# Optimization experiments

Measured on AMD Instinct MI355X. Metric: run time of the kernel, lower is better.

The kernel has to match this reference:

```python
import jax, jax.numpy as jnp
import numpy as np

B, D, H, Q, N, V = 2048, 2048, 16, 128, 8192, 128


def setup_inputs() -> dict:
    key = jax.random.key(0)
    k1, k2, k3, k4, k5 = jax.random.split(key, 5)
    return {
        "x": jax.random.normal(k1, (B, D), dtype=jnp.float32),
        "keys": jax.random.normal(k2, (N, Q), dtype=jnp.float32),
        "values": jax.random.normal(k3, (N, V), dtype=jnp.float32),
        "Wq": jax.random.normal(k4, (H * Q, D), dtype=jnp.float32) * (1.0 / np.sqrt(D)),
        "Wo": jax.random.normal(k5, (D, H * V), dtype=jnp.float32) * (1.0 / np.sqrt(H * V)),
    }


def reference(x, keys, values, Wq, Wo):
    b = x.shape[0]
    h, q = H, Q
    # queries: [B, H, Q]
    queries = (x @ Wq.T).reshape(b, h, q)
    # einsum 'aib,ajb->aijb' then sum over last axis == dot product over Q
    scores = jnp.einsum('bhq,nq->bhn', queries, keys) / jnp.sqrt(jnp.asarray(q, x.dtype))
    attn = jax.nn.softmax(scores, axis=-1)  # [B, H, N]
    # Original: einsum('aib,ajc->aijc', attn, values) sums attn over its N axis
    # (label b) independently of values' N axis (label j), giving
    # out[a,i,j,c] = attn_rowsum[a,i] * values[j,c]; mean over j then yields
    # attn_rowsum[a,i] * mean_n(values)[c]. Computed here without the [B,H,N,V]
    # intermediate (mathematically identical).
    attn_rowsum = attn.sum(axis=-1)        # [B, H] (== 1 up to fp error)
    vmean = values.mean(axis=0)            # [V]
    outv = (attn_rowsum[:, :, None] * vmean[None, None, :]).reshape(b, -1)  # [B, H*V]
    return outv @ Wo.T + x
```

## Files before the change

kernel.cpp:

```cpp
#include <hip/hip_runtime.h>


#define NROWS 8192
#define VDIM  128
#define DDIM  2048
#define BDIM  2048

__global__ void __launch_bounds__(256) colsum_kernel(
    const float4* __restrict__ vals4,
    float4* __restrict__ partial4)
{
    __shared__ float4 s[256];
    const int t = threadIdx.x;
    const int bid = blockIdx.x;
    float4 acc = make_float4(0.f, 0.f, 0.f, 0.f);
    const int base = bid * 4096;
#pragma unroll
    for (int j = 0; j < 16; ++j) {
        float4 v = vals4[base + t + 256 * j];
        acc.x += v.x; acc.y += v.y; acc.z += v.z; acc.w += v.w;
    }
    s[t] = acc;
    __syncthreads();
    if (t < 32) {
        float4 r = s[t];
#pragma unroll
        for (int k = 1; k < 8; ++k) {
            float4 v = s[t + 32 * k];
            r.x += v.x; r.y += v.y; r.z += v.z; r.w += v.w;
        }
        partial4[bid * 32 + t] = r;
    }
}

__global__ void __launch_bounds__(256) c_kernel(
    const float4* __restrict__ partial4,
    const float4* __restrict__ Wo4,
    float4* __restrict__ cvec4)
{
    __shared__ float4 s[256];
    __shared__ float4 vm_lds[32];
    const int t = threadIdx.x;
    const int d0 = blockIdx.x * 4;

    float4 w[4][2];
#pragma unroll
    for (int r = 0; r < 4; ++r) {
        const float4* row = Wo4 + (size_t)(d0 + r) * 512;
        w[r][0] = row[t];
        w[r][1] = row[t + 256];
    }

    float4 acc = make_float4(0.f, 0.f, 0.f, 0.f);
#pragma unroll
    for (int j = 0; j < 8; ++j) {
        float4 v = partial4[t + 256 * j];
        acc.x += v.x; acc.y += v.y; acc.z += v.z; acc.w += v.w;
    }
    s[t] = acc;
    __syncthreads();
    if (t < 32) {
        float4 r = s[t];
#pragma unroll
        for (int k = 1; k < 8; ++k) {
            float4 v = s[t + 32 * k];
            r.x += v.x; r.y += v.y; r.z += v.z; r.w += v.w;
        }
        const float inv = 1.0f / (float)NROWS;
        r.x *= inv; r.y *= inv; r.z *= inv; r.w *= inv;
        vm_lds[t] = r;
    }
    __syncthreads();

    const float4 vm = vm_lds[t & 31];
    float4 dots;
    {
        float* dp = (float*)&dots;
#pragma unroll
        for (int r = 0; r < 4; ++r) {
            float4 a = w[r][0], b = w[r][1];
            a.x += b.x; a.y += b.y; a.z += b.z; a.w += b.w;
            dp[r] = a.x * vm.x + a.y * vm.y + a.z * vm.z + a.w * vm.w;
        }
    }
    s[t] = dots;
    __syncthreads();

    if (t < 64) {
        float4 r = s[t];
#pragma unroll
        for (int k = 1; k < 4; ++k) {
            float4 v = s[t + 64 * k];
            r.x += v.x; r.y += v.y; r.z += v.z; r.w += v.w;
        }
#pragma unroll
        for (int off = 32; off; off >>= 1) {
            r.x += __shfl_down(r.x, off);
            r.y += __shfl_down(r.y, off);
            r.z += __shfl_down(r.z, off);
            r.w += __shfl_down(r.w, off);
        }
        if (t == 0) cvec4[blockIdx.x] = r;
    }
}

__global__ void __launch_bounds__(256) add_kernel(
    const float4* __restrict__ x4,
    const float* __restrict__ cvec,
    float4* __restrict__ out4)
{
    const float4* __restrict__ c4 = (const float4*)cvec;
    const int t = threadIdx.x;
    const size_t base = (size_t)blockIdx.x * 512 + t;
    float4 xv0 = x4[base];
    float4 xv1 = x4[base + 256];
    float4 cv0 = c4[t];
    float4 cv1 = c4[t + 256];
    xv0.x += cv0.x; xv0.y += cv0.y; xv0.z += cv0.z; xv0.w += cv0.w;
    xv1.x += cv1.x; xv1.y += cv1.y; xv1.z += cv1.z; xv1.w += cv1.w;
    out4[base] = xv0;
    out4[base + 256] = xv1;
}

extern "C" void kernel_launch(void* const* d_in, const int* in_sizes, int n_in,
                              void* d_out, int out_size, void* d_ws, size_t ws_size,
                              hipStream_t stream) {
    const float4* vals4 = (const float4*)d_in[2];
    const float4* Wo4   = (const float4*)d_in[4];
    const float4* x4    = (const float4*)d_in[0];
    float4* out4 = (float4*)d_out;
    char* ws = (char*)d_ws;

    float4* partial4 = (float4*)ws;
    float4* cvec4    = (float4*)(ws + 32768);

    colsum_kernel<<<64, 256, 0, stream>>>(vals4, partial4);
    c_kernel<<<512, 256, 0, stream>>>(partial4, Wo4, cvec4);
    add_kernel<<<2048, 256, 0, stream>>>(x4, (const float*)cvec4, out4);
}
```

Baseline: 19.92 us.

## Rebalance grid sizes across kernels and use nontemporal loads/stores for streams

Doubles the colsum blocks (128 blocks of 2048 float4) and c_kernel blocks (each now computing two output rows instead of four). Each add_kernel block now covers two rows, halving its grid. Wo and x are read, and the output written, with nontemporal builtins so single-use streams bypass cache retention. The aim is more parallelism in the small reduction kernels and less cache pollution in the bandwidth-bound add. The cost is more redundant partial-sum reads per c_kernel block.

```diff
diff --git a/kernel.cpp b/kernel.cpp
--- a/kernel.cpp
+++ b/kernel.cpp
@@ -5,6 +5,18 @@
 #define VDIM  128
 #define DDIM  2048
 #define BDIM  2048
+#define PB    128
+
+typedef float nf4 __attribute__((ext_vector_type(4)));
+
+__device__ __forceinline__ float4 nt_load4(const float4* p) {
+    nf4 v = __builtin_nontemporal_load((const nf4*)p);
+    return make_float4(v.x, v.y, v.z, v.w);
+}
+__device__ __forceinline__ void nt_store4(float4 v, float4* p) {
+    nf4 n = {v.x, v.y, v.z, v.w};
+    __builtin_nontemporal_store(n, (nf4*)p);
+}
 
 __global__ void __launch_bounds__(256) colsum_kernel(
     const float4* __restrict__ vals4,
@@ -14,9 +26,9 @@
     const int t = threadIdx.x;
     const int bid = blockIdx.x;
     float4 acc = make_float4(0.f, 0.f, 0.f, 0.f);
-    const int base = bid * 4096;
+    const int base = bid * 2048;
 #pragma unroll
-    for (int j = 0; j < 16; ++j) {
+    for (int j = 0; j < 8; ++j) {
         float4 v = vals4[base + t + 256 * j];
         acc.x += v.x; acc.y += v.y; acc.z += v.z; acc.w += v.w;
     }
@@ -36,24 +48,25 @@
 __global__ void __launch_bounds__(256) c_kernel(
     const float4* __restrict__ partial4,
     const float4* __restrict__ Wo4,
-    float4* __restrict__ cvec4)
+    float2* __restrict__ cvec2)
 {
     __shared__ float4 s[256];
+    __shared__ float2 s2[256];
     __shared__ float4 vm_lds[32];
     const int t = threadIdx.x;
-    const int d0 = blockIdx.x * 4;
+    const int d0 = blockIdx.x * 2;
 
-    float4 w[4][2];
+    float4 w[2][2];
 #pragma unroll
-    for (int r = 0; r < 4; ++r) {
+    for (int r = 0; r < 2; ++r) {
         const float4* row = Wo4 + (size_t)(d0 + r) * 512;
-        w[r][0] = row[t];
-        w[r][1] = row[t + 256];
+        w[r][0] = nt_load4(&row[t]);
+        w[r][1] = nt_load4(&row[t + 256]);
     }
 
     float4 acc = make_float4(0.f, 0.f, 0.f, 0.f);
 #pragma unroll
-    for (int j = 0; j < 8; ++j) {
+    for (int j = 0; j < 16; ++j) {
         float4 v = partial4[t + 256 * j];
         acc.x += v.x; acc.y += v.y; acc.z += v.z; acc.w += v.w;
     }
@@ -73,34 +86,30 @@
     __syncthreads();
 
     const float4 vm = vm_lds[t & 31];
-    float4 dots;
-    {
-        float* dp = (float*)&dots;
+    float2 dots;
 #pragma unroll
-        for (int r = 0; r < 4; ++r) {
-            float4 a = w[r][0], b = w[r][1];
-            a.x += b.x; a.y += b.y; a.z += b.z; a.w += b.w;
-            dp[r] = a.x * vm.x + a.y * vm.y + a.z * vm.z + a.w * vm.w;
-        }
+    for (int r = 0; r < 2; ++r) {
+        float4 a = w[r][0], b = w[r][1];
+        a.x += b.x; a.y += b.y; a.z += b.z; a.w += b.w;
+        float dv = a.x * vm.x + a.y * vm.y + a.z * vm.z + a.w * vm.w;
+        if (r == 0) dots.x = dv; else dots.y = dv;
     }
-    s[t] = dots;
+    s2[t] = dots;
     __syncthreads();
 
     if (t < 64) {
-        float4 r = s[t];
+        float2 r = s2[t];
 #pragma unroll
         for (int k = 1; k < 4; ++k) {
-            float4 v = s[t + 64 * k];
-            r.x += v.x; r.y += v.y; r.z += v.z; r.w += v.w;
+            float2 v = s2[t + 64 * k];
+            r.x += v.x; r.y += v.y;
         }
 #pragma unroll
         for (int off = 32; off; off >>= 1) {
             r.x += __shfl_down(r.x, off);
             r.y += __shfl_down(r.y, off);
-            r.z += __shfl_down(r.z, off);
-            r.w += __shfl_down(r.w, off);
         }
-        if (t == 0) cvec4[blockIdx.x] = r;
+        if (t == 0) cvec2[blockIdx.x] = r;
     }
 }
 
@@ -111,15 +120,21 @@
 {
     const float4* __restrict__ c4 = (const float4*)cvec;
     const int t = threadIdx.x;
-    const size_t base = (size_t)blockIdx.x * 512 + t;
-    float4 xv0 = x4[base];
-    float4 xv1 = x4[base + 256];
+    const size_t base = (size_t)blockIdx.x * 1024 + t;
+    float4 xv0 = nt_load4(&x4[base]);
+    float4 xv1 = nt_load4(&x4[base + 256]);
+    float4 xv2 = nt_load4(&x4[base + 512]);
+    float4 xv3 = nt_load4(&x4[base + 768]);
     float4 cv0 = c4[t];
     float4 cv1 = c4[t + 256];
     xv0.x += cv0.x; xv0.y += cv0.y; xv0.z += cv0.z; xv0.w += cv0.w;
     xv1.x += cv1.x; xv1.y += cv1.y; xv1.z += cv1.z; xv1.w += cv1.w;
-    out4[base] = xv0;
-    out4[base + 256] = xv1;
+    xv2.x += cv0.x; xv2.y += cv0.y; xv2.z += cv0.z; xv2.w += cv0.w;
+    xv3.x += cv1.x; xv3.y += cv1.y; xv3.z += cv1.z; xv3.w += cv1.w;
+    nt_store4(xv0, &out4[base]);
+    nt_store4(xv1, &out4[base + 256]);
+    nt_store4(xv2, &out4[base + 512]);
+    nt_store4(xv3, &out4[base + 768]);
 }
 
 extern "C" void kernel_launch(void* const* d_in, const int* in_sizes, int n_in,
@@ -132,9 +147,9 @@
     char* ws = (char*)d_ws;
 
     float4* partial4 = (float4*)ws;
-    float4* cvec4    = (float4*)(ws + 32768);
+    float2* cvec2    = (float2*)(ws + 65536);
 
-    colsum_kernel<<<64, 256, 0, stream>>>(vals4, partial4);
-    c_kernel<<<512, 256, 0, stream>>>(partial4, Wo4, cvec4);
-    add_kernel<<<2048, 256, 0, stream>>>(x4, (const float*)cvec4, out4);
+    colsum_kernel<<<PB, 256, 0, stream>>>(vals4, partial4);
+    c_kernel<<<1024, 256, 0, stream>>>(partial4, Wo4, cvec2);
+    add_kernel<<<1024, 256, 0, stream>>>(x4, (const float*)cvec2, out4);
 }
```

After: 21.64 us. 8.7% more time.
